# Optimization experiments

Hardware: AMD Instinct MI355X
Metric: run time of the kernel (lower is better)

## Reference

```python
import jax, jax.numpy as jnp
import numpy as np

N_NODES, N_EDGES, N_GRAPHS = 100000, 800000, 64
X_DIM, E_DIM, U_DIM, H = 128, 64, 128, 128
BN_EPS = 1e-5


def _bn(x, gamma, beta):
    # BatchNorm1d, training mode: biased batch stats over dim 0
    m = x.mean(axis=0)
    v = x.var(axis=0)
    return (x - m) * jax.lax.rsqrt(v + BN_EPS) * gamma + beta


def _mlp(x, Wa, ba, g, be, Wb, bb):
    h = jax.nn.selu(_bn(x @ Wa + ba, g, be))
    return h @ Wb + bb


def setup_inputs() -> dict:
    key = jax.random.key(0)
    ks = jax.random.split(key, 10)
    x = jax.random.normal(ks[0], (N_NODES, X_DIM), jnp.float32)
    edge_attr = jax.random.normal(ks[1], (N_EDGES, E_DIM), jnp.float32)
    u = jax.random.normal(ks[2], (N_GRAPHS, U_DIM), jnp.float32)
    edge_index = jax.random.randint(ks[3], (2, N_EDGES), 0, N_NODES, jnp.int32)
    batch = jnp.sort(jax.random.randint(ks[4], (N_NODES,), 0, N_GRAPHS, jnp.int32))

    def lin(k, fan_in, fan_out):
        return jax.random.normal(k, (fan_in, fan_out), jnp.float32) / np.sqrt(fan_in)

    return {
        "x": x, "edge_attr": edge_attr, "u": u,
        "W1a": lin(ks[5], X_DIM + E_DIM, H), "b1a": jnp.zeros(H),
        "g1": jnp.ones(H), "be1": jnp.zeros(H),
        "W1b": lin(ks[6], H, H), "b1b": jnp.zeros(H),
        "W2a": lin(ks[7], X_DIM + H + U_DIM, H), "b2a": jnp.zeros(H),
        "g2": jnp.ones(H), "be2": jnp.zeros(H),
        "W2b": lin(ks[8], H, H), "b2b": jnp.zeros(H),
        "edge_index": edge_index, "batch": batch,
    }


def reference(x, edge_attr, u, W1a, b1a, g1, be1, W1b, b1b,
              W2a, b2a, g2, be2, W2b, b2b, edge_index, batch):
    row, col = edge_index[0], edge_index[1]
    n = x.shape[0]
    # gather source node feats, run edge MLP
    out = jnp.concatenate([x[row], edge_attr], axis=1)        # [E, X+Ed]
    out = _mlp(out, W1a, b1a, g1, be1, W1b, b1b)              # [E, H]
    # scatter-mean over destination nodes
    s = jax.ops.segment_sum(out, col, num_segments=n)         # [N, H]
    cnt = jax.ops.segment_sum(jnp.ones((out.shape[0], 1), out.dtype), col,
                              num_segments=n)
    agg = s / jnp.maximum(cnt, 1.0)
    # node update MLP
    out2 = jnp.concatenate([x, agg, u[batch]], axis=1)        # [N, X+H+U]
    return _mlp(out2, W2a, b2a, g2, be2, W2b, b2b)
```

## Files before the change

### kernel.cpp

```cpp
#include <hip/hip_runtime.h>
#include <hip/hip_bf16.h>
#include <math.h>


typedef __attribute__((ext_vector_type(8))) short bfrag;
typedef __attribute__((ext_vector_type(4))) float f32x4;
typedef __attribute__((ext_vector_type(4))) float f4raw;
typedef __attribute__((ext_vector_type(2))) unsigned u32x2;

#define N_EDGES 800000
#define N_NODES 100000
#define BN_EPS 1e-5f

static __device__ __forceinline__ short f2bf(float f) {
    union { float f; unsigned u; } v; v.f = f;
    unsigned r = (v.u + 0x7FFFu + ((v.u >> 16) & 1u)) >> 16;
    return (short)r;
}
static __device__ __forceinline__ float bf2f(short h) {
    union { unsigned u; float f; } v;
    v.u = ((unsigned)(unsigned short)h) << 16;
    return v.f;
}
static __device__ __forceinline__ unsigned pack2(float lo, float hi) {
    return ((unsigned)(unsigned short)f2bf(lo)) | (((unsigned)(unsigned short)f2bf(hi)) << 16);
}

static __device__ __forceinline__ bfrag load8f_bf(const float* __restrict__ p) {
    float4 a = *(const float4*)p;
    float4 b = *(const float4*)(p + 4);
    bfrag r;
    r[0] = f2bf(a.x); r[1] = f2bf(a.y); r[2] = f2bf(a.z); r[3] = f2bf(a.w);
    r[4] = f2bf(b.x); r[5] = f2bf(b.y); r[6] = f2bf(b.z); r[7] = f2bf(b.w);
    return r;
}
static __device__ __forceinline__ bfrag load8f_bf_nt(const float* __restrict__ p) {
    f4raw a = __builtin_nontemporal_load((const f4raw*)p);
    f4raw b = __builtin_nontemporal_load((const f4raw*)(p + 4));
    bfrag r;
    r[0] = f2bf(a[0]); r[1] = f2bf(a[1]); r[2] = f2bf(a[2]); r[3] = f2bf(a[3]);
    r[4] = f2bf(b[0]); r[5] = f2bf(b[1]); r[6] = f2bf(b[2]); r[7] = f2bf(b[3]);
    return r;
}
static __device__ __forceinline__ u32x2 ldnt_u2(const short* p) {
    return __builtin_nontemporal_load((const u32x2*)p);
}
static __device__ __forceinline__ void stnt_frag(short* p, bfrag v) {
    __builtin_nontemporal_store(v, (bfrag*)p);
}

static __device__ __forceinline__ float selu_f(float v) {
    return v > 0.f ? 1.0507009873554805f * v
                   : 1.7580993408473766f * (__expf(v) - 1.0f);
}

static __device__ __forceinline__ void pack_slot(short* __restrict__ Wp, int k, int n, float val) {
    int kb = k >> 5, g = (k >> 3) & 3, j = k & 7;
    Wp[(((size_t)kb * 128 + n) * 4 + g) * 8 + j] = f2bf(val);
}

__global__ void prep(const float* __restrict__ W1a, const float* __restrict__ W1b,
                     const float* __restrict__ b1b, const float* __restrict__ W2a,
                     const float* __restrict__ W2b,
                     short* __restrict__ Wp1x, short* __restrict__ Wp1e,
                     short* __restrict__ Wp2a, short* __restrict__ Wp2b,
                     float* __restrict__ cb,
                     const int* __restrict__ colI, int* __restrict__ CNTi, int E)
{
    const int b = blockIdx.x, t = threadIdx.x;
    if (b < 64) {
        int idx = b * 256 + t; int k = idx >> 7, n = idx & 127;
        pack_slot(Wp1x, k, n, W1a[idx]);
    } else if (b < 96) {
        int idx = (b - 64) * 256 + t; int k = idx >> 7, n = idx & 127;
        pack_slot(Wp1e, k, n, W1a[128 * 128 + idx]);
    } else if (b < 160) {
        int idx = (b - 96) * 256 + t; int k = idx >> 7, n = idx & 127;
        pack_slot(Wp2a, k, n, W2a[idx]);
    } else if (b < 224) {
        int idx = (b - 160) * 256 + t; int k = idx >> 7, n = idx & 127;
        int kt = ((k & 7) << 4) + (k >> 3);
        float s = 0.f;
        for (int j = 0; j < 128; ++j)
            s += W1b[kt * 128 + j] * W2a[(size_t)(128 + j) * 128 + n];
        pack_slot(Wp2a + 16384, k, n, s);
    } else if (b < 288) {
        int idx = (b - 224) * 256 + t; int k = idx >> 7, n = idx & 127;
        pack_slot(Wp2a + 32768, k, n, W2a[(size_t)256 * 128 + idx]);
    } else if (b < 352) {
        int idx = (b - 288) * 256 + t; int k = idx >> 7, n = idx & 127;
        int kt = ((k & 7) << 4) + (k >> 3);
        pack_slot(Wp2b, k, n, W2b[(size_t)kt * 128 + n]);
    } else if (b == 352) {
        if (t < 128) {
            float s = 0.f;
            for (int j = 0; j < 128; ++j) s += b1b[j] * W2a[(size_t)(128 + j) * 128 + t];
            cb[t] = s;
        }
    } else {
        int e = (b - 353) * 256 + t;
        if (e < E) atomicAdd(&CNTi[colI[e]], 1);
    }
}

__global__ void scan1(const int* __restrict__ cnt, int* __restrict__ off,
                      int* __restrict__ bsum, int N) {
    __shared__ int ls[1024];
    int i = blockIdx.x * 1024 + threadIdx.x;
    int v = (i < N) ? cnt[i] : 0;
    ls[threadIdx.x] = v;
    __syncthreads();
    for (int d = 1; d < 1024; d <<= 1) {
        int t = (threadIdx.x >= d) ? ls[threadIdx.x - d] : 0;
        __syncthreads();
        ls[threadIdx.x] += t;
        __syncthreads();
    }
    if (i < N) off[i] = ls[threadIdx.x] - v;
    if (threadIdx.x == 1023) bsum[blockIdx.x] = ls[1023];
}

__global__ void scan2(const int* __restrict__ bsum, int* __restrict__ boff, int NB) {
    __shared__ int ls[128];
    int v = (threadIdx.x < NB) ? bsum[threadIdx.x] : 0;
    ls[threadIdx.x] = v;
    __syncthreads();
    for (int d = 1; d < 128; d <<= 1) {
        int t = (threadIdx.x >= d) ? ls[threadIdx.x - d] : 0;
        __syncthreads();
        ls[threadIdx.x] += t;
        __syncthreads();
    }
    if (threadIdx.x < NB) boff[threadIdx.x] = ls[threadIdx.x] - v;
}

__global__ void scan3(int* __restrict__ off, const int* __restrict__ boff, int N) {
    int i = blockIdx.x * 1024 + threadIdx.x;
    if (i < N) off[i] += boff[blockIdx.x];
}

__global__ void fill_k(const int* __restrict__ col, int* __restrict__ off,
                       int* __restrict__ spos, int E) {
    int e = blockIdx.x * 256 + threadIdx.x;
    if (e < E) spos[e] = atomicAdd(&off[col[e]], 1);
}

__global__ __launch_bounds__(256) void gemmX(
    const float* __restrict__ x, const short* __restrict__ Wp,
    short* __restrict__ Xap, int N)
{
    const int lane = threadIdx.x & 63, wave = threadIdx.x >> 6;
    const int m0 = blockIdx.x * 128 + wave * 32;
    if (m0 >= N) return;
    const int lr = lane & 15, lg = lane >> 4;
    const int v0 = m0 + lr, v1 = m0 + 16 + lr;

    f32x4 acc[2][8];
#pragma unroll
    for (int t = 0; t < 2; ++t)
#pragma unroll
        for (int n = 0; n < 8; ++n) acc[t][n] = (f32x4){0.f, 0.f, 0.f, 0.f};

#pragma unroll
    for (int kb = 0; kb < 4; ++kb) {
        bfrag a0 = load8f_bf(x + (size_t)v0 * 128 + kb * 32 + lg * 8);
        bfrag a1 = load8f_bf(x + (size_t)v1 * 128 + kb * 32 + lg * 8);
        const short* wb = Wp + (size_t)kb * 4096;
#pragma unroll
        for (int n0 = 0; n0 < 8; ++n0) {
            bfrag b = *(const bfrag*)(wb + ((n0 * 16 + lr) * 4 + lg) * 8);
            acc[0][n0] = __builtin_amdgcn_mfma_f32_16x16x32_bf16(a0, b, acc[0][n0], 0, 0, 0);
            acc[1][n0] = __builtin_amdgcn_mfma_f32_16x16x32_bf16(a1, b, acc[1][n0], 0, 0, 0);
        }
    }
#pragma unroll
    for (int t = 0; t < 2; ++t) {
        const int rbase = m0 + t * 16 + lg * 4;
#pragma unroll
        for (int r = 0; r < 4; ++r) {
            bfrag o;
#pragma unroll
            for (int n0 = 0; n0 < 8; ++n0) o[n0] = f2bf(acc[t][n0][r]);
            *(bfrag*)(Xap + (size_t)(rbase + r) * 128 + lr * 8) = o;
        }
    }
}

__global__ __launch_bounds__(256) void gemm1n(
    const float* __restrict__ ea, const int* __restrict__ rowI,
    const int* __restrict__ SPOS, const short* __restrict__ Wp,
    const short* __restrict__ Xap, short* __restrict__ T1p,
    float* __restrict__ stats, int E)
{
    const int lane = threadIdx.x & 63, wave = threadIdx.x >> 6;
    const int lr = lane & 15, lg = lane >> 4;

    float ps[8], qs[8];
#pragma unroll
    for (int n0 = 0; n0 < 8; ++n0) { ps[n0] = 0.f; qs[n0] = 0.f; }

    const int NT = E >> 7;
    for (int tile = blockIdx.x; tile < NT; tile += gridDim.x) {
        const int m0 = tile * 128 + wave * 32;

        int spos[2][4];
        bfrag xa[2][4];
#pragma unroll
        for (int t = 0; t < 2; ++t) {
            const int rbase = m0 + t * 16 + lg * 4;
#pragma unroll
            for (int r = 0; r < 4; ++r) {
                const int e = rbase + r;
                spos[t][r] = SPOS[e];
                xa[t][r] = *(const bfrag*)(Xap + (size_t)rowI[e] * 128 + lr * 8);
            }
        }

        const float* er0 = ea + (size_t)(m0 + lr) * 64;
        const float* er1 = ea + (size_t)(m0 + 16 + lr) * 64;

        f32x4 acc[2][8];
#pragma unroll
        for (int t = 0; t < 2; ++t)
#pragma unroll
            for (int n = 0; n < 8; ++n) acc[t][n] = (f32x4){0.f, 0.f, 0.f, 0.f};

#pragma unroll
        for (int kb = 0; kb < 2; ++kb) {
            bfrag a0 = load8f_bf_nt(er0 + kb * 32 + lg * 8);
            bfrag a1 = load8f_bf_nt(er1 + kb * 32 + lg * 8);
            const short* wb = Wp + (size_t)kb * 4096;
#pragma unroll
            for (int n0 = 0; n0 < 8; ++n0) {
                bfrag b = *(const bfrag*)(wb + ((n0 * 16 + lr) * 4 + lg) * 8);
                acc[0][n0] = __builtin_amdgcn_mfma_f32_16x16x32_bf16(a0, b, acc[0][n0], 0, 0, 0);
                acc[1][n0] = __builtin_amdgcn_mfma_f32_16x16x32_bf16(a1, b, acc[1][n0], 0, 0, 0);
            }
        }

#pragma unroll
        for (int t = 0; t < 2; ++t) {
#pragma unroll
            for (int r = 0; r < 4; ++r) {
                bfrag o;
#pragma unroll
                for (int n0 = 0; n0 < 8; ++n0) {
                    float v = acc[t][n0][r] + bf2f(xa[t][r][n0]);
                    ps[n0] += v; qs[n0] += v * v;
                    o[n0] = f2bf(v);
                }
                stnt_frag(T1p + (size_t)spos[t][r] * 128 + lr * 8, o);
            }
        }
    }

    __shared__ float ls[256];
    ls[threadIdx.x] = 0.f;
    __syncthreads();
#pragma unroll
    for (int n0 = 0; n0 < 8; ++n0) {
        const int c = n0 * 16 + lr;
        float p = ps[n0], q = qs[n0];
        p += __shfl_xor(p, 16); p += __shfl_xor(p, 32);
        q += __shfl_xor(q, 16); q += __shfl_xor(q, 32);
        if (lg == 0) { atomicAdd(&ls[c], p); atomicAdd(&ls[128 + c], q); }
    }
    __syncthreads();
    atomicAdd(&stats[threadIdx.x], ls[threadIdx.x]);
}

__global__ __launch_bounds__(256) void segsel(
    const short* __restrict__ T1p, const float* __restrict__ stats,
    const float* __restrict__ g1, const float* __restrict__ be1,
    const int* __restrict__ OFF, const int* __restrict__ CNTi,
    short* __restrict__ Aggm, int N, float invR)
{
    __shared__ float ls_sc[128], ls_sh[128];
    if (threadIdx.x < 128) {
        int p = threadIdx.x;
        int c = ((p & 7) << 4) + (p >> 3);
        float mean = stats[c] * invR;
        float var = stats[128 + c] * invR - mean * mean;
        float sc = g1[c] * rsqrtf(var + BN_EPS);
        ls_sc[p] = sc;
        ls_sh[p] = be1[c] - mean * sc;
    }
    __syncthreads();

    const int lane = threadIdx.x & 63;
    const int h = lane >> 5, t = lane & 31;
    const int wid = blockIdx.x * 4 + (threadIdx.x >> 6);
    const int nw = gridDim.x * 4;
    const int chunk = (N + nw - 1) / nw;
    const int v0 = wid * chunk;
    const int v1 = (v0 + chunk < N) ? v0 + chunk : N;

    const float sc0 = ls_sc[t * 4 + 0], sc1 = ls_sc[t * 4 + 1];
    const float sc2 = ls_sc[t * 4 + 2], sc3 = ls_sc[t * 4 + 3];
    const float sh0 = ls_sh[t * 4 + 0], sh1 = ls_sh[t * 4 + 1];
    const float sh2 = ls_sh[t * 4 + 2], sh3 = ls_sh[t * 4 + 3];

    for (int v = v0; v < v1; ++v) {
        const int cnt = CNTi[v];
        const int beg = OFF[v] - cnt;
        const short* base = T1p + (size_t)beg * 128 + t * 4;
        float a0 = 0.f, a1 = 0.f, a2 = 0.f, a3 = 0.f;
        int j = 0;
        for (; j + 4 <= cnt; j += 4) {
            u32x2 wA = ldnt_u2(base + (size_t)(j + h) * 128);
            u32x2 wB = ldnt_u2(base + (size_t)(j + 2 + h) * 128);
            a0 += selu_f(sc0 * bf2f((short)(wA[0] & 0xffff)) + sh0);
            a1 += selu_f(sc1 * bf2f((short)(wA[0] >> 16)) + sh1);
            a2 += selu_f(sc2 * bf2f((short)(wA[1] & 0xffff)) + sh2);
            a3 += selu_f(sc3 * bf2f((short)(wA[1] >> 16)) + sh3);
            a0 += selu_f(sc0 * bf2f((short)(wB[0] & 0xffff)) + sh0);
            a1 += selu_f(sc1 * bf2f((short)(wB[0] >> 16)) + sh1);
            a2 += selu_f(sc2 * bf2f((short)(wB[1] & 0xffff)) + sh2);
            a3 += selu_f(sc3 * bf2f((short)(wB[1] >> 16)) + sh3);
        }
        for (; j < cnt; j += 2) {
            if (j + h < cnt) {
                u32x2 w = ldnt_u2(base + (size_t)(j + h) * 128);
                a0 += selu_f(sc0 * bf2f((short)(w[0] & 0xffff)) + sh0);
                a1 += selu_f(sc1 * bf2f((short)(w[0] >> 16)) + sh1);
                a2 += selu_f(sc2 * bf2f((short)(w[1] & 0xffff)) + sh2);
                a3 += selu_f(sc3 * bf2f((short)(w[1] >> 16)) + sh3);
            }
        }
        a0 += __shfl_xor(a0, 32); a1 += __shfl_xor(a1, 32);
        a2 += __shfl_xor(a2, 32); a3 += __shfl_xor(a3, 32);
        if (h == 0) {
            const float inv = 1.0f / fmaxf((float)cnt, 1.0f);
            u32x2 o;
            o[0] = pack2(a0 * inv, a1 * inv);
            o[1] = pack2(a2 * inv, a3 * inv);
            *(u32x2*)(Aggm + (size_t)v * 128 + t * 4) = o;
        }
    }
}

__global__ __launch_bounds__(256) void gemm3_node(
    const float* __restrict__ x, const short* __restrict__ Aggm,
    const float* __restrict__ u, const int* __restrict__ batch,
    const int* __restrict__ CNTi, const float* __restrict__ cb,
    const short* __restrict__ Wp, short* __restrict__ T2p,
    float* __restrict__ stats, int N)
{
    const int lane = threadIdx.x & 63, wave = threadIdx.x >> 6;
    const int m0 = blockIdx.x * 128 + wave * 32;
    const bool active = (m0 < N);
    const int lr = lane & 15, lg = lane >> 4;
    __shared__ float ls[256];
    ls[threadIdx.x] = 0.f;
    __syncthreads();

    if (active) {
        const int v0 = m0 + lr, v1 = m0 + 16 + lr;
        const float* u0 = u + (size_t)batch[v0] * 128;
        const float* u1 = u + (size_t)batch[v1] * 128;

        f32x4 acc[2][8];
#pragma unroll
        for (int t = 0; t < 2; ++t)
#pragma unroll
            for (int n = 0; n < 8; ++n) acc[t][n] = (f32x4){0.f, 0.f, 0.f, 0.f};

#pragma unroll
        for (int kb = 0; kb < 12; ++kb) {
            bfrag a0, a1;
            if (kb >= 4 && kb < 8) {
                a0 = *(const bfrag*)(Aggm + (size_t)v0 * 128 + (kb - 4) * 32 + lg * 8);
                a1 = *(const bfrag*)(Aggm + (size_t)v1 * 128 + (kb - 4) * 32 + lg * 8);
            } else {
                const float *p0, *p1;
                if (kb < 4) {
                    p0 = x + (size_t)v0 * 128 + kb * 32 + lg * 8;
                    p1 = x + (size_t)v1 * 128 + kb * 32 + lg * 8;
                } else {
                    p0 = u0 + (kb - 8) * 32 + lg * 8;
                    p1 = u1 + (kb - 8) * 32 + lg * 8;
                }
                a0 = load8f_bf(p0);
                a1 = load8f_bf(p1);
            }
            const short* wb = Wp + (size_t)kb * 4096;
#pragma unroll
            for (int n0 = 0; n0 < 8; ++n0) {
                bfrag b = *(const bfrag*)(wb + ((n0 * 16 + lr) * 4 + lg) * 8);
                acc[0][n0] = __builtin_amdgcn_mfma_f32_16x16x32_bf16(a0, b, acc[0][n0], 0, 0, 0);
                acc[1][n0] = __builtin_amdgcn_mfma_f32_16x16x32_bf16(a1, b, acc[1][n0], 0, 0, 0);
            }
        }
        float cbl[8];
#pragma unroll
        for (int n0 = 0; n0 < 8; ++n0) cbl[n0] = cb[n0 * 16 + lr];
        float ps[8], qs[8];
#pragma unroll
        for (int n0 = 0; n0 < 8; ++n0) { ps[n0] = 0.f; qs[n0] = 0.f; }
#pragma unroll
        for (int t = 0; t < 2; ++t) {
            const int rbase = m0 + t * 16 + lg * 4;
            float fl[4];
#pragma unroll
            for (int r = 0; r < 4; ++r) fl[r] = (CNTi[rbase + r] > 0) ? 1.f : 0.f;
#pragma unroll
            for (int r = 0; r < 4; ++r) {
                bfrag o;
#pragma unroll
                for (int n0 = 0; n0 < 8; ++n0) {
                    float v = acc[t][n0][r] + fl[r] * cbl[n0];
                    ps[n0] += v; qs[n0] += v * v;
                    o[n0] = f2bf(v);
                }
                *(bfrag*)(T2p + (size_t)(rbase + r) * 128 + lr * 8) = o;
            }
        }
#pragma unroll
        for (int n0 = 0; n0 < 8; ++n0) {
            const int c = n0 * 16 + lr;
            float p = ps[n0], q = qs[n0];
            p += __shfl_xor(p, 16); p += __shfl_xor(p, 32);
            q += __shfl_xor(q, 16); q += __shfl_xor(q, 32);
            if (lg == 0) { atomicAdd(&ls[c], p); atomicAdd(&ls[128 + c], q); }
        }
    }
    __syncthreads();
    atomicAdd(&stats[threadIdx.x], ls[threadIdx.x]);
}

__global__ __launch_bounds__(256) void gemm4_node(
    const short* __restrict__ T2p, const float* __restrict__ stats,
    const float* __restrict__ g2, const float* __restrict__ be2,
    const short* __restrict__ Wp, const float* __restrict__ b2b,
    float* __restrict__ out, int N, float invR)
{
    __shared__ float ls_sc[128], ls_sh[128];
    if (threadIdx.x < 128) {
        int c = threadIdx.x;
        float mean = stats[c] * invR;
        float var = stats[128 + c] * invR - mean * mean;
        float sc = g2[c] * rsqrtf(var + BN_EPS);
        ls_sc[c] = sc;
        ls_sh[c] = be2[c] - mean * sc;
    }
    __syncthreads();

    const int lane = threadIdx.x & 63, wave = threadIdx.x >> 6;
    const int m0 = blockIdx.x * 128 + wave * 32;
    if (m0 >= N) return;
    const int lr = lane & 15, lg = lane >> 4;
    const int e0 = m0 + lr, e1 = m0 + 16 + lr;

    f32x4 acc[2][8];
#pragma unroll
    for (int n0 = 0; n0 < 8; ++n0) {
        float bias = b2b[n0 * 16 + lr];
        acc[0][n0] = (f32x4){bias, bias, bias, bias};
        acc[1][n0] = (f32x4){bias, bias, bias, bias};
    }
#pragma unroll
    for (int kb = 0; kb < 4; ++kb) {
        float scl[8], shf[8];
#pragma unroll
        for (int j = 0; j < 8; ++j) {
            int c = j * 16 + kb * 4 + lg;
            scl[j] = ls_sc[c];
            shf[j] = ls_sh[c];
        }
        bfrag r0 = *(const bfrag*)(T2p + (size_t)e0 * 128 + kb * 32 + lg * 8);
        bfrag r1 = *(const bfrag*)(T2p + (size_t)e1 * 128 + kb * 32 + lg * 8);
        bfrag a0, a1;
#pragma unroll
        for (int j = 0; j < 8; ++j) {
            a0[j] = f2bf(selu_f(bf2f(r0[j]) * scl[j] + shf[j]));
            a1[j] = f2bf(selu_f(bf2f(r1[j]) * scl[j] + shf[j]));
        }
        const short* wb = Wp + (size_t)kb * 4096;
#pragma unroll
        for (int n0 = 0; n0 < 8; ++n0) {
            bfrag b = *(const bfrag*)(wb + ((n0 * 16 + lr) * 4 + lg) * 8);
            acc[0][n0] = __builtin_amdgcn_mfma_f32_16x16x32_bf16(a0, b, acc[0][n0], 0, 0, 0);
            acc[1][n0] = __builtin_amdgcn_mfma_f32_16x16x32_bf16(a1, b, acc[1][n0], 0, 0, 0);
        }
    }
#pragma unroll
    for (int t = 0; t < 2; ++t) {
        const int rbase = m0 + t * 16 + lg * 4;
#pragma unroll
        for (int n0 = 0; n0 < 8; ++n0) {
            const int c = n0 * 16 + lr;
#pragma unroll
            for (int r = 0; r < 4; ++r)
                __builtin_nontemporal_store(acc[t][n0][r],
                    out + (size_t)(rbase + r) * 128 + c);
        }
    }
}

extern "C" void kernel_launch(void* const* d_in, const int* in_sizes, int n_in,
                              void* d_out, int out_size, void* d_ws, size_t ws_size,
                              hipStream_t stream)
{
    const float* x   = (const float*)d_in[0];
    const float* ea  = (const float*)d_in[1];
    const float* u   = (const float*)d_in[2];
    const float* W1a = (const float*)d_in[3];
    const float* g1  = (const float*)d_in[5];
    const float* be1 = (const float*)d_in[6];
    const float* W1b = (const float*)d_in[7];
    const float* b1b = (const float*)d_in[8];
    const float* W2a = (const float*)d_in[9];
    const float* g2  = (const float*)d_in[11];
    const float* be2 = (const float*)d_in[12];
    const float* W2b = (const float*)d_in[13];
    const float* b2b = (const float*)d_in[14];
    const int* ei    = (const int*)d_in[15];
    const int* rowI  = ei;
    const int* colI  = ei + N_EDGES;
    const int* batch = (const int*)d_in[16];
    float* out = (float*)d_out;

    if (ws_size < 260252416ull) return;

    char* ws = (char*)d_ws;
    short* Wp1x   = (short*)(ws + 0);
    short* Wp1e   = (short*)(ws + 32768);
    short* Wp2a   = (short*)(ws + 49152);
    short* Wp2b   = (short*)(ws + 147456);
    float* cb     = (float*)(ws + 245760);
    float* stats1 = (float*)(ws + 246272);
    float* stats2 = (float*)(ws + 247296);
    int*   CNTi   = (int*)(ws + 250368);
    int*   OFF    = (int*)(ws + 650368);
    int*   BSUM   = (int*)(ws + 1050368);
    int*   BOFF   = (int*)(ws + 1051392);
    int*   SPOS   = (int*)(ws + 1052416);
    short* Aggm   = (short*)(ws + 4252416);
    short* Xap    = (short*)(ws + 29852416ull);
    short* T2p    = (short*)(ws + 29852416ull);
    short* T1p    = (short*)(ws + 55452416ull);

    hipMemsetAsync(stats1, 0, 2048, stream);
    hipMemsetAsync(CNTi, 0, 400000, stream);

    prep<<<353 + (N_EDGES + 255) / 256, 256, 0, stream>>>(
        W1a, W1b, b1b, W2a, W2b, Wp1x, Wp1e, Wp2a, Wp2b, cb, colI, CNTi, N_EDGES);

    scan1<<<98, 1024, 0, stream>>>(CNTi, OFF, BSUM, N_NODES);
    scan2<<<1, 128, 0, stream>>>(BSUM, BOFF, 98);
    scan3<<<98, 1024, 0, stream>>>(OFF, BOFF, N_NODES);
    fill_k<<<(N_EDGES + 255) / 256, 256, 0, stream>>>(colI, OFF, SPOS, N_EDGES);

    gemmX<<<(N_NODES + 127) / 128, 256, 0, stream>>>(x, Wp1x, Xap, N_NODES);

    gemm1n<<<2048, 256, 0, stream>>>(ea, rowI, SPOS, Wp1e, Xap, T1p, stats1, N_EDGES);

    segsel<<<2048, 256, 0, stream>>>(T1p, stats1, g1, be1, OFF, CNTi, Aggm,
                                     N_NODES, 1.0f / (float)N_EDGES);

    gemm3_node<<<(N_NODES + 127) / 128, 256, 0, stream>>>(x, Aggm, u, batch, CNTi, cb,
                                                          Wp2a, T2p, stats2, N_NODES);
    gemm4_node<<<(N_NODES + 127) / 128, 256, 0, stream>>>(T2p, stats2, g2, be2, Wp2b, b2b,
                                                          out, N_NODES, 1.0f / (float)N_NODES);
}
```

Measured before the change: 370.7 us.

## Fuse three-pass scan into one kernel, fold stats memset, widen segsel loads

Replaces the scan1/scan2/scan3 chain with a single kernel in which each block re-reduces all preceding counts to get its base offset. The stats1 memset is moved into an extra block of fill_k. Together these cut two launches and a memset call. The segment-reduce kernel now has each lane load 16-byte bf16 fragments covering 8 channels over 4 rows per wave, with a two-step shuffle reduction, which means fewer, wider loads per edge. The trade-offs are redundant prefix reads in the later scan blocks (O(N) per block) and a possibly less even load balance for low-degree nodes.

```diff
diff --git a/kernel.cpp b/kernel.cpp
--- a/kernel.cpp
+++ b/kernel.cpp
@@ -6,7 +6,6 @@
 typedef __attribute__((ext_vector_type(8))) short bfrag;
 typedef __attribute__((ext_vector_type(4))) float f32x4;
 typedef __attribute__((ext_vector_type(4))) float f4raw;
-typedef __attribute__((ext_vector_type(2))) unsigned u32x2;
 
 #define N_EDGES 800000
 #define N_NODES 100000
@@ -21,9 +20,6 @@
     union { unsigned u; float f; } v;
     v.u = ((unsigned)(unsigned short)h) << 16;
     return v.f;
-}
-static __device__ __forceinline__ unsigned pack2(float lo, float hi) {
-    return ((unsigned)(unsigned short)f2bf(lo)) | (((unsigned)(unsigned short)f2bf(hi)) << 16);
 }
 
 static __device__ __forceinline__ bfrag load8f_bf(const float* __restrict__ p) {
@@ -42,8 +38,8 @@
     r[4] = f2bf(b[0]); r[5] = f2bf(b[1]); r[6] = f2bf(b[2]); r[7] = f2bf(b[3]);
     return r;
 }
-static __device__ __forceinline__ u32x2 ldnt_u2(const short* p) {
-    return __builtin_nontemporal_load((const u32x2*)p);
+static __device__ __forceinline__ bfrag ldnt_frag(const short* p) {
+    return __builtin_nontemporal_load((const bfrag*)p);
 }
 static __device__ __forceinline__ void stnt_frag(short* p, bfrag v) {
     __builtin_nontemporal_store(v, (bfrag*)p);
@@ -103,44 +99,41 @@
     }
 }
 
-__global__ void scan1(const int* __restrict__ cnt, int* __restrict__ off,
-                      int* __restrict__ bsum, int N) {
+__global__ __launch_bounds__(1024) void scanF(const int* __restrict__ cnt,
+                                              int* __restrict__ off, int N) {
     __shared__ int ls[1024];
-    int i = blockIdx.x * 1024 + threadIdx.x;
+    const int b = blockIdx.x, tid = threadIdx.x;
+    int s = 0;
+    const int lim = b * 1024;
+    for (int i = tid; i < lim; i += 1024) s += cnt[i];
+    ls[tid] = s;
+    __syncthreads();
+    for (int d = 512; d > 0; d >>= 1) {
+        if (tid < d) ls[tid] += ls[tid + d];
+        __syncthreads();
+    }
+    const int base = ls[0];
+    __syncthreads();
+    const int i = lim + tid;
     int v = (i < N) ? cnt[i] : 0;
-    ls[threadIdx.x] = v;
+    ls[tid] = v;
     __syncthreads();
     for (int d = 1; d < 1024; d <<= 1) {
-        int t = (threadIdx.x >= d) ? ls[threadIdx.x - d] : 0;
+        int t = (tid >= d) ? ls[tid - d] : 0;
         __syncthreads();
-        ls[threadIdx.x] += t;
+        ls[tid] += t;
         __syncthreads();
     }
-    if (i < N) off[i] = ls[threadIdx.x] - v;
-    if (threadIdx.x == 1023) bsum[blockIdx.x] = ls[1023];
-}
-
-__global__ void scan2(const int* __restrict__ bsum, int* __restrict__ boff, int NB) {
-    __shared__ int ls[128];
-    int v = (threadIdx.x < NB) ? bsum[threadIdx.x] : 0;
-    ls[threadIdx.x] = v;
-    __syncthreads();
-    for (int d = 1; d < 128; d <<= 1) {
-        int t = (threadIdx.x >= d) ? ls[threadIdx.x - d] : 0;
-        __syncthreads();
-        ls[threadIdx.x] += t;
-        __syncthreads();
-    }
-    if (threadIdx.x < NB) boff[threadIdx.x] = ls[threadIdx.x] - v;
-}
-
-__global__ void scan3(int* __restrict__ off, const int* __restrict__ boff, int N) {
-    int i = blockIdx.x * 1024 + threadIdx.x;
-    if (i < N) off[i] += boff[blockIdx.x];
+    if (i < N) off[i] = base + ls[tid] - v;
 }
 
 __global__ void fill_k(const int* __restrict__ col, int* __restrict__ off,
-                       int* __restrict__ spos, int E) {
+                       int* __restrict__ spos, float* __restrict__ statsz, int E) {
+    if (blockIdx.x == gridDim.x - 1) {
+        statsz[threadIdx.x] = 0.f;
+        statsz[256 + threadIdx.x] = 0.f;
+        return;
+    }
     int e = blockIdx.x * 256 + threadIdx.x;
     if (e < E) spos[e] = atomicAdd(&off[col[e]], 1);
 }
@@ -288,53 +281,55 @@
     __syncthreads();
 
     const int lane = threadIdx.x & 63;
-    const int h = lane >> 5, t = lane & 31;
+    const int q = lane & 15, rp = lane >> 4;
     const int wid = blockIdx.x * 4 + (threadIdx.x >> 6);
     const int nw = gridDim.x * 4;
     const int chunk = (N + nw - 1) / nw;
     const int v0 = wid * chunk;
     const int v1 = (v0 + chunk < N) ? v0 + chunk : N;
 
-    const float sc0 = ls_sc[t * 4 + 0], sc1 = ls_sc[t * 4 + 1];
-    const float sc2 = ls_sc[t * 4 + 2], sc3 = ls_sc[t * 4 + 3];
-    const float sh0 = ls_sh[t * 4 + 0], sh1 = ls_sh[t * 4 + 1];
-    const float sh2 = ls_sh[t * 4 + 2], sh3 = ls_sh[t * 4 + 3];
+    float sc8[8], sh8[8];
+#pragma unroll
+    for (int i = 0; i < 8; ++i) { sc8[i] = ls_sc[q * 8 + i]; sh8[i] = ls_sh[q * 8 + i]; }
 
     for (int v = v0; v < v1; ++v) {
         const int cnt = CNTi[v];
         const int beg = OFF[v] - cnt;
-        const short* base = T1p + (size_t)beg * 128 + t * 4;
-        float a0 = 0.f, a1 = 0.f, a2 = 0.f, a3 = 0.f;
+        const short* base = T1p + (size_t)beg * 128 + q * 8;
+        float a[8];
+#pragma unroll
+        for (int i = 0; i < 8; ++i) a[i] = 0.f;
         int j = 0;
+        for (; j + 8 <= cnt; j += 8) {
+            bfrag w0 = ldnt_frag(base + (size_t)(j + rp) * 128);
+            bfrag w1 = ldnt_frag(base + (size_t)(j + 4 + rp) * 128);
+#pragma unroll
+            for (int i = 0; i < 8; ++i) {
+                a[i] += selu_f(sc8[i] * bf2f(w0[i]) + sh8[i]);
+                a[i] += selu_f(sc8[i] * bf2f(w1[i]) + sh8[i]);
+            }
+        }
         for (; j + 4 <= cnt; j += 4) {
-            u32x2 wA = ldnt_u2(base + (size_t)(j + h) * 128);
-            u32x2 wB = ldnt_u2(base + (size_t)(j + 2 + h) * 128);
-            a0 += selu_f(sc0 * bf2f((short)(wA[0] & 0xffff)) + sh0);
-            a1 += selu_f(sc1 * bf2f((short)(wA[0] >> 16)) + sh1);
-            a2 += selu_f(sc2 * bf2f((short)(wA[1] & 0xffff)) + sh2);
-            a3 += selu_f(sc3 * bf2f((short)(wA[1] >> 16)) + sh3);
-            a0 += selu_f(sc0 * bf2f((short)(wB[0] & 0xffff)) + sh0);
-            a1 += selu_f(sc1 * bf2f((short)(wB[0] >> 16)) + sh1);
-            a2 += selu_f(sc2 * bf2f((short)(wB[1] & 0xffff)) + sh2);
-            a3 += selu_f(sc3 * bf2f((short)(wB[1] >> 16)) + sh3);
-        }
-        for (; j < cnt; j += 2) {
-            if (j + h < cnt) {
-                u32x2 w = ldnt_u2(base + (size_t)(j + h) * 128);
-                a0 += selu_f(sc0 * bf2f((short)(w[0] & 0xffff)) + sh0);
-                a1 += selu_f(sc1 * bf2f((short)(w[0] >> 16)) + sh1);
-                a2 += selu_f(sc2 * bf2f((short)(w[1] & 0xffff)) + sh2);
-                a3 += selu_f(sc3 * bf2f((short)(w[1] >> 16)) + sh3);
-            }
-        }
-        a0 += __shfl_xor(a0, 32); a1 += __shfl_xor(a1, 32);
-        a2 += __shfl_xor(a2, 32); a3 += __shfl_xor(a3, 32);
-        if (h == 0) {
+            bfrag w = ldnt_frag(base + (size_t)(j + rp) * 128);
+#pragma unroll
+            for (int i = 0; i < 8; ++i) a[i] += selu_f(sc8[i] * bf2f(w[i]) + sh8[i]);
+        }
+        if (j + rp < cnt) {
+            bfrag w = ldnt_frag(base + (size_t)(j + rp) * 128);
+#pragma unroll
+            for (int i = 0; i < 8; ++i) a[i] += selu_f(sc8[i] * bf2f(w[i]) + sh8[i]);
+        }
+#pragma unroll
+        for (int i = 0; i < 8; ++i) {
+            a[i] += __shfl_xor(a[i], 16);
+            a[i] += __shfl_xor(a[i], 32);
+        }
+        if (rp == 0) {
             const float inv = 1.0f / fmaxf((float)cnt, 1.0f);
-            u32x2 o;
-            o[0] = pack2(a0 * inv, a1 * inv);
-            o[1] = pack2(a2 * inv, a3 * inv);
-            *(u32x2*)(Aggm + (size_t)v * 128 + t * 4) = o;
+            bfrag o;
+#pragma unroll
+            for (int i = 0; i < 8; ++i) o[i] = f2bf(a[i] * inv);
+            *(bfrag*)(Aggm + (size_t)v * 128 + q * 8) = o;
         }
     }
 }
@@ -532,24 +527,19 @@
     float* stats2 = (float*)(ws + 247296);
     int*   CNTi   = (int*)(ws + 250368);
     int*   OFF    = (int*)(ws + 650368);
-    int*   BSUM   = (int*)(ws + 1050368);
-    int*   BOFF   = (int*)(ws + 1051392);
     int*   SPOS   = (int*)(ws + 1052416);
     short* Aggm   = (short*)(ws + 4252416);
     short* Xap    = (short*)(ws + 29852416ull);
     short* T2p    = (short*)(ws + 29852416ull);
     short* T1p    = (short*)(ws + 55452416ull);
 
-    hipMemsetAsync(stats1, 0, 2048, stream);
     hipMemsetAsync(CNTi, 0, 400000, stream);
 
     prep<<<353 + (N_EDGES + 255) / 256, 256, 0, stream>>>(
         W1a, W1b, b1b, W2a, W2b, Wp1x, Wp1e, Wp2a, Wp2b, cb, colI, CNTi, N_EDGES);
 
-    scan1<<<98, 1024, 0, stream>>>(CNTi, OFF, BSUM, N_NODES);
-    scan2<<<1, 128, 0, stream>>>(BSUM, BOFF, 98);
-    scan3<<<98, 1024, 0, stream>>>(OFF, BOFF, N_NODES);
-    fill_k<<<(N_EDGES + 255) / 256, 256, 0, stream>>>(colI, OFF, SPOS, N_EDGES);
+    scanF<<<98, 1024, 0, stream>>>(CNTi, OFF, N_NODES);
+    fill_k<<<(N_EDGES + 255) / 256 + 1, 256, 0, stream>>>(colI, OFF, SPOS, stats1, N_EDGES);
 
     gemmX<<<(N_NODES + 127) / 128, 256, 0, stream>>>(x, Wp1x, Xap, N_NODES);
 
```

New measurement: 378.4 us. +2.1%, slower.
